# Kernel tuning notes

Measured on AMD Instinct MI355X. Metric: run time of the kernel, lower is better.

The kernel has to match this reference:

```python
import jax, jax.numpy as jnp
import numpy as np

# Config mirroring pooler_config / set_config
INPUT_LEN = 8192
POOLED_LEN = 512
DEPTH = 4            # log2(INPUT_LEN / POOLED_LEN)
BASE = 2.0           # base > 0 branch
FLIP_RIGHT = True
SORT_BACK = True
EMB_DEPTH = 768
BATCH = 8


def _pool_one(emb, score):
    """emb: [L, E], score: [L] -> ([L/2**DEPTH, E], [L/2**DEPTH]).
    One iterative sort-fold-merge chain (the per-batch our_topk)."""
    for _ in range(DEPTH):
        half = score.shape[0] // 2
        # descending sort indices (torch sort(descending=True).indices)
        sort_idx = jnp.argsort(-score)
        left = sort_idx[:half]
        right = sort_idx[half:]
        if FLIP_RIGHT:
            right = right[::-1]
        pairs = jnp.stack([left, right])            # [2, half]
        sc = score[pairs]                           # [2, half]
        # softmax over the pair dimension of base**score
        w = jax.nn.softmax(jnp.power(BASE, sc), axis=0)  # [2, half]
        score = (sc * w).sum(axis=0)                # [half]
        emb = (emb[pairs] * w[:, :, None]).sum(axis=0)   # [half, E]
        if SORT_BACK:
            # reorder merged tokens back to original order of the top (left) indices
            order = jnp.argsort(left)
            score = score[order]
            emb = emb[order]
    return emb, score


def setup_inputs() -> dict:
    key = jax.random.key(0)
    k1, k2 = jax.random.split(key)
    embs = jax.random.normal(k1, (BATCH, INPUT_LEN, EMB_DEPTH), dtype=jnp.float32)
    scores = jax.random.normal(k2, (BATCH, INPUT_LEN, 1), dtype=jnp.float32)
    return {"embs": embs, "scores": scores}


def reference(embs, scores):
    # inputs already at INPUT_LEN, so pad_to_input_len is an identity;
    # scores is squeezed from [B, L, 1] to [B, L]
    new_embs, new_scores = jax.vmap(_pool_one)(embs, scores[..., 0])
    return new_embs, new_scores
```

## Files before the change

kernel.cpp:

```cpp
#include <hip/hip_runtime.h>
#include <stdint.h>

#define BATCH   8
#define LEN0    8192
#define EMB     768
#define POOLED  512
#define NJC     16
#define PL      (BATCH * LEN0)

struct __align__(16) Rec { uint32_t iA, iB; float w0, w1; };


__device__ __forceinline__ float npy_expf(float x) {
    const float q = rintf(__fmul_rn(x, 1.44269504088896341f));
    float r = __fmaf_rn(q, -0.693359375f, x);
    r = __fmaf_rn(q, 2.12194440e-4f, r);
    const float r2 = __fmul_rn(r, r);
    float p = 1.9875691500E-4f;
    p = __fmaf_rn(p, r, 1.3981999507E-3f);
    p = __fmaf_rn(p, r, 8.3334519073E-3f);
    p = __fmaf_rn(p, r, 4.1665795894E-2f);
    p = __fmaf_rn(p, r, 1.6666665459E-1f);
    p = __fmaf_rn(p, r, 5.0000001201E-1f);
    p = __fmaf_rn(p, r2, r);
    p = __fadd_rn(p, 1.0f);
    const int qi = (int)q;
    const float sc = __uint_as_float((uint32_t)((qi + 127) << 23));
    return __fmul_rn(p, sc);
}

__global__ __launch_bounds__(256) void k_rank(const float* __restrict__ sc,
                                              uint16_t* __restrict__ rankp,
                                              int L, int C) {
    __shared__ float keys[512];
    const int b     = blockIdx.z;
    const int jc    = blockIdx.y;
    const int base  = b * LEN0;
    const int ibase = blockIdx.x * 1024;
    const int jb    = jc * C;
    const int tid   = threadIdx.x;

    for (int j = tid; j < C; j += 256)
        keys[j] = sc[base + jb + j];
    __syncthreads();

    const int i0 = ibase + tid * 4;
    const float4 mev = *(const float4*)&sc[base + i0];
    const float me[4] = {mev.x, mev.y, mev.z, mev.w};
    uint32_t cnt[4] = {0, 0, 0, 0};
    if (jb + C <= ibase) {
        for (int j = 0; j < C; j += 4) {
            const float4 kv = *(const float4*)&keys[j];
            #pragma unroll
            for (int m = 0; m < 4; m++)
                cnt[m] += (kv.x >= me[m]) + (kv.y >= me[m]) +
                          (kv.z >= me[m]) + (kv.w >= me[m]);
        }
    } else if (jb >= ibase + 1024) {
        for (int j = 0; j < C; j += 4) {
            const float4 kv = *(const float4*)&keys[j];
            #pragma unroll
            for (int m = 0; m < 4; m++)
                cnt[m] += (kv.x > me[m]) + (kv.y > me[m]) +
                          (kv.z > me[m]) + (kv.w > me[m]);
        }
    } else {
        for (int j = 0; j < C; j += 4) {
            const float4 kv = *(const float4*)&keys[j];
            const int jj = jb + j;
            #pragma unroll
            for (int m = 0; m < 4; m++) {
                const int i = i0 + m;
                cnt[m] += ((kv.x > me[m]) || (kv.x == me[m] && (jj    ) < i))
                        + ((kv.y > me[m]) || (kv.y == me[m] && (jj + 1) < i))
                        + ((kv.z > me[m]) || (kv.z == me[m] && (jj + 2) < i))
                        + ((kv.w > me[m]) || (kv.w == me[m] && (jj + 3) < i));
            }
        }
    }
    *(ushort4*)&rankp[(size_t)jc * PL + base + i0] =
        make_ushort4((uint16_t)cnt[0], (uint16_t)cnt[1],
                     (uint16_t)cnt[2], (uint16_t)cnt[3]);
}

__global__ __launch_bounds__(256) void k_sumscatter(const uint16_t* __restrict__ rankp,
                                                    uint16_t* __restrict__ rank16,
                                                    uint16_t* __restrict__ ior16,
                                                    uint32_t* __restrict__ csum,
                                                    int L) {
    __shared__ uint32_t part[256];
    const int b    = blockIdx.y;
    const int base = b * LEN0;
    const int c    = blockIdx.x;
    const int tid  = threadIdx.x;
    const int i    = c * 256 + tid;

    uint32_t r = 0;
    #pragma unroll
    for (int pl = 0; pl < NJC; pl++)
        r += rankp[(size_t)pl * PL + base + i];
    rank16[base + i] = (uint16_t)r;
    ior16[base + r] = (uint16_t)i;

    const uint32_t half = (uint32_t)(L / 2);
    uint32_t flag = (r < half) ? 1u : 0u;
    part[tid] = flag;
    __syncthreads();
    for (int off = 128; off > 0; off >>= 1) {
        if (tid < off) part[tid] += part[tid + off];
        __syncthreads();
    }
    if (tid == 0) csum[b * 32 + c] = part[0];
}

__global__ __launch_bounds__(256) void k_pairx(const float* __restrict__ sc_cur,
                                               float* __restrict__ sc_nxt,
                                               const uint16_t* __restrict__ rank16,
                                               const uint16_t* __restrict__ ior16,
                                               const uint32_t* __restrict__ csum,
                                               Rec* __restrict__ rec,
                                               int L) {
    __shared__ uint32_t cs[32];
    __shared__ uint32_t part[256];
    const int b    = blockIdx.y;
    const int base = b * LEN0;
    const int c    = blockIdx.x;
    const int tid  = threadIdx.x;
    const int i    = c * 256 + tid;
    const uint32_t half = (uint32_t)(L / 2);

    if (tid < c) cs[tid] = csum[b * 32 + tid];
    const uint32_t r = rank16[base + i];
    const uint32_t flag = (r < half) ? 1u : 0u;
    part[tid] = flag;
    __syncthreads();

    uint32_t dstBase = 0;
    for (int t = 0; t < c; t++) dstBase += cs[t];

    for (int off = 1; off < 256; off <<= 1) {
        uint32_t v = part[tid];
        uint32_t add = (tid >= off) ? part[tid - off] : 0u;
        __syncthreads();
        part[tid] = v + add;
        __syncthreads();
    }
    if (!flag) return;
    const uint32_t dst = dstBase + part[tid] - 1u;

    const uint32_t p = ior16[base + (uint32_t)(L - 1) - r];
    const float s0 = sc_cur[base + i];
    const float s1 = sc_cur[base + p];
    const float p0 = (float)exp2((double)s0);
    const float p1 = (float)exp2((double)s1);
    const float mx = fmaxf(p0, p1);
    const float d0 = __fsub_rn(p0, mx);
    const float d1 = __fsub_rn(p1, mx);
    const float e0 = npy_expf(d0);
    const float e1 = npy_expf(d1);
    const float den = __fadd_rn(e0, e1);
    const float w0 = __fdiv_rn(e0, den);
    const float w1 = __fdiv_rn(e1, den);
    sc_nxt[base + dst] = __fadd_rn(__fmul_rn(s0, w0), __fmul_rn(s1, w1));

    Rec rc; rc.iA = (uint32_t)i; rc.iB = p; rc.w0 = w0; rc.w1 = w1;
    rec[(size_t)b * half + dst] = rc;
}

__global__ __launch_bounds__(192)
void k_merge(const float* __restrict__ emb,
             const Rec* __restrict__ rec0, const Rec* __restrict__ rec1,
             const Rec* __restrict__ rec2, const Rec* __restrict__ rec3,
             const float* __restrict__ sc_fin, float* __restrict__ out) {
    __shared__ uint32_t sl[2][16];
    __shared__ float    sw[2][16];
    const int s = blockIdx.x;
    const int b = blockIdx.y;
    const int d = threadIdx.x;

    if (d == 0) {
        const Rec r = rec3[b * 512 + s];
        sl[0][0] = r.iA; sl[0][1] = r.iB;
        sw[0][0] = r.w0; sw[0][1] = r.w1;
    }
    __syncthreads();
    if (d < 2) {
        const Rec r = rec2[b * 1024 + sl[0][d]];
        sl[1][2*d] = r.iA; sl[1][2*d+1] = r.iB;
        sw[1][2*d]   = __fmul_rn(sw[0][d], r.w0);
        sw[1][2*d+1] = __fmul_rn(sw[0][d], r.w1);
    }
    __syncthreads();
    if (d < 4) {
        const Rec r = rec1[b * 2048 + sl[1][d]];
        sl[0][2*d] = r.iA; sl[0][2*d+1] = r.iB;
        sw[0][2*d]   = __fmul_rn(sw[1][d], r.w0);
        sw[0][2*d+1] = __fmul_rn(sw[1][d], r.w1);
    }
    __syncthreads();
    if (d < 8) {
        const Rec r = rec0[b * 4096 + sl[0][d]];
        sl[1][2*d] = r.iA; sl[1][2*d+1] = r.iB;
        sw[1][2*d]   = __fmul_rn(sw[0][d], r.w0);
        sw[1][2*d+1] = __fmul_rn(sw[0][d], r.w1);
    }
    __syncthreads();

    const float* ebase = emb + (size_t)b * LEN0 * EMB;
    float4 acc = make_float4(0.f, 0.f, 0.f, 0.f);
    #pragma unroll
    for (int k = 0; k < 16; k++) {
        const float4 v = *(const float4*)(ebase + (size_t)sl[1][k] * EMB + d * 4);
        const float wk = sw[1][k];
        acc.x += wk * v.x; acc.y += wk * v.y; acc.z += wk * v.z; acc.w += wk * v.w;
    }
    *(float4*)(out + ((size_t)b * POOLED + s) * EMB + d * 4) = acc;
    if (d == 0)
        out[(size_t)BATCH * POOLED * EMB + b * POOLED + s] = sc_fin[b * LEN0 + s];
}

extern "C" void kernel_launch(void* const* d_in, const int* in_sizes, int n_in,
                              void* d_out, int out_size, void* d_ws, size_t ws_size,
                              hipStream_t stream) {
    const float* embs   = (const float*)d_in[0];
    const float* scores = (const float*)d_in[1];
    float* out = (float*)d_out;
    char* ws = (char*)d_ws;

    float*    scA    = (float*)(ws + 0x000000);
    float*    scB    = (float*)(ws + 0x040000);
    uint16_t* rank16 = (uint16_t*)(ws + 0x080000);
    uint16_t* ior16  = (uint16_t*)(ws + 0x0A0000);
    Rec*      rec0   = (Rec*)(ws + 0x0C0000);
    Rec*      rec1   = (Rec*)(ws + 0x140000);
    Rec*      rec2   = (Rec*)(ws + 0x180000);
    Rec*      rec3   = (Rec*)(ws + 0x1A0000);
    uint16_t* rankp  = (uint16_t*)(ws + 0x1C0000);
    uint32_t* csum   = (uint32_t*)(ws + 0x3C0000);

    const float* sc_in[4]  = {scores, scA, scB, scA};
    float*       sc_out[4] = {scA, scB, scA, scB};
    Rec*         recs[4]   = {rec0, rec1, rec2, rec3};

    int L = LEN0;
    for (int l = 0; l < 4; l++) {
        const int C = L / NJC;
        k_rank<<<dim3(L / 1024, NJC, BATCH), 256, 0, stream>>>(sc_in[l], rankp, L, C);
        k_sumscatter<<<dim3(L / 256, BATCH), 256, 0, stream>>>(rankp, rank16, ior16, csum, L);
        k_pairx<<<dim3(L / 256, BATCH), 256, 0, stream>>>(sc_in[l], sc_out[l],
                                                          rank16, ior16, csum, recs[l], L);
        L >>= 1;
    }

    k_merge<<<dim3(POOLED, BATCH), 192, 0, stream>>>(embs, rec0, rec1, rec2, rec3,
                                                     scB, out);
}
```

Measured before the change: 177.0 us.

## Fuse rank counting and sum-scatter into one full-row shared-memory kernel

Replaces the split rank-partial kernel plus the separate summation/scatter kernel with a templated kernel per level. Each 1024-thread block loads the whole score row into LDS, splits the comparison work across thread groups, and reduces the partial counts in shared memory before writing rank, inverse index and chunk sums. This removes the global rankp round trip and one launch per level. The cost is a redundant full-row load per block, a large LDS footprint that limits occupancy, and a fixed grid of 32 blocks per batch at every level.

```diff
diff --git a/kernel.cpp b/kernel.cpp
--- a/kernel.cpp
+++ b/kernel.cpp
@@ -5,8 +5,6 @@
 #define LEN0    8192
 #define EMB     768
 #define POOLED  512
-#define NJC     16
-#define PL      (BATCH * LEN0)
 
 struct __align__(16) Rec { uint32_t iA, iB; float w0, w1; };
 
@@ -29,35 +27,45 @@
     return __fmul_rn(p, sc);
 }
 
-__global__ __launch_bounds__(256) void k_rank(const float* __restrict__ sc,
-                                              uint16_t* __restrict__ rankp,
-                                              int L, int C) {
-    __shared__ float keys[512];
-    const int b     = blockIdx.z;
-    const int jc    = blockIdx.y;
+template<int L>
+__global__ __launch_bounds__(1024) void k_rankfull(const float* __restrict__ sc,
+                                                   uint16_t* __restrict__ rank16,
+                                                   uint16_t* __restrict__ ior16,
+                                                   uint32_t* __restrict__ csum) {
+    constexpr int IC = L / 32;
+    constexpr int IQ = IC / 4;
+    constexpr int G  = 1024 / IQ;
+    constexpr int JR = L / G;
+    __shared__ float    keys[L];
+    __shared__ uint16_t partial[4096];
+    __shared__ uint32_t wsum[16];
+    const int b     = blockIdx.y;
     const int base  = b * LEN0;
-    const int ibase = blockIdx.x * 1024;
-    const int jb    = jc * C;
+    const int ibase = blockIdx.x * IC;
     const int tid   = threadIdx.x;
 
-    for (int j = tid; j < C; j += 256)
-        keys[j] = sc[base + jb + j];
-    __syncthreads();
-
-    const int i0 = ibase + tid * 4;
-    const float4 mev = *(const float4*)&sc[base + i0];
+    for (int e = tid * 4; e < L; e += 4096)
+        *(float4*)&keys[e] = *(const float4*)&sc[base + e];
+    __syncthreads();
+
+    const int iq  = tid % IQ;
+    const int g   = tid / IQ;
+    const int i0  = ibase + iq * 4;
+    const int jlo = g * JR;
+    const float4 mev = *(const float4*)&keys[i0];
     const float me[4] = {mev.x, mev.y, mev.z, mev.w};
+
     uint32_t cnt[4] = {0, 0, 0, 0};
-    if (jb + C <= ibase) {
-        for (int j = 0; j < C; j += 4) {
+    if (jlo + JR <= i0) {
+        for (int j = jlo; j < jlo + JR; j += 4) {
             const float4 kv = *(const float4*)&keys[j];
             #pragma unroll
             for (int m = 0; m < 4; m++)
                 cnt[m] += (kv.x >= me[m]) + (kv.y >= me[m]) +
                           (kv.z >= me[m]) + (kv.w >= me[m]);
         }
-    } else if (jb >= ibase + 1024) {
-        for (int j = 0; j < C; j += 4) {
+    } else if (jlo >= i0 + 4) {
+        for (int j = jlo; j < jlo + JR; j += 4) {
             const float4 kv = *(const float4*)&keys[j];
             #pragma unroll
             for (int m = 0; m < 4; m++)
@@ -65,52 +73,46 @@
                           (kv.z > me[m]) + (kv.w > me[m]);
         }
     } else {
-        for (int j = 0; j < C; j += 4) {
+        for (int j = jlo; j < jlo + JR; j += 4) {
             const float4 kv = *(const float4*)&keys[j];
-            const int jj = jb + j;
             #pragma unroll
             for (int m = 0; m < 4; m++) {
                 const int i = i0 + m;
-                cnt[m] += ((kv.x > me[m]) || (kv.x == me[m] && (jj    ) < i))
-                        + ((kv.y > me[m]) || (kv.y == me[m] && (jj + 1) < i))
-                        + ((kv.z > me[m]) || (kv.z == me[m] && (jj + 2) < i))
-                        + ((kv.w > me[m]) || (kv.w == me[m] && (jj + 3) < i));
+                cnt[m] += ((kv.x > me[m]) || (kv.x == me[m] && (j    ) < i))
+                        + ((kv.y > me[m]) || (kv.y == me[m] && (j + 1) < i))
+                        + ((kv.z > me[m]) || (kv.z == me[m] && (j + 2) < i))
+                        + ((kv.w > me[m]) || (kv.w == me[m] && (j + 3) < i));
             }
         }
     }
-    *(ushort4*)&rankp[(size_t)jc * PL + base + i0] =
+    *(ushort4*)&partial[g * IC + iq * 4] =
         make_ushort4((uint16_t)cnt[0], (uint16_t)cnt[1],
                      (uint16_t)cnt[2], (uint16_t)cnt[3]);
-}
-
-__global__ __launch_bounds__(256) void k_sumscatter(const uint16_t* __restrict__ rankp,
-                                                    uint16_t* __restrict__ rank16,
-                                                    uint16_t* __restrict__ ior16,
-                                                    uint32_t* __restrict__ csum,
-                                                    int L) {
-    __shared__ uint32_t part[256];
-    const int b    = blockIdx.y;
-    const int base = b * LEN0;
-    const int c    = blockIdx.x;
-    const int tid  = threadIdx.x;
-    const int i    = c * 256 + tid;
-
-    uint32_t r = 0;
+    __syncthreads();
+
+    uint32_t flag = 0;
+    if (tid < IC) {
+        uint32_t r = 0;
+        #pragma unroll 4
+        for (int gg = 0; gg < G; gg++)
+            r += partial[gg * IC + tid];
+        const int i = ibase + tid;
+        rank16[base + i] = (uint16_t)r;
+        ior16[base + r] = (uint16_t)i;
+        flag = (r < (uint32_t)(L / 2)) ? 1u : 0u;
+    }
     #pragma unroll
-    for (int pl = 0; pl < NJC; pl++)
-        r += rankp[(size_t)pl * PL + base + i];
-    rank16[base + i] = (uint16_t)r;
-    ior16[base + r] = (uint16_t)i;
-
-    const uint32_t half = (uint32_t)(L / 2);
-    uint32_t flag = (r < half) ? 1u : 0u;
-    part[tid] = flag;
-    __syncthreads();
-    for (int off = 128; off > 0; off >>= 1) {
-        if (tid < off) part[tid] += part[tid + off];
-        __syncthreads();
-    }
-    if (tid == 0) csum[b * 32 + c] = part[0];
+    for (int off = 32; off > 0; off >>= 1)
+        flag += __shfl_down(flag, off, 64);
+    if ((tid & 63) == 0) wsum[tid >> 6] = flag;
+    __syncthreads();
+    if (tid == 0) {
+        uint32_t s = 0;
+        constexpr int NW = (IC + 63) / 64;
+        #pragma unroll
+        for (int w = 0; w < NW; w++) s += wsum[w];
+        csum[b * 32 + blockIdx.x] = s;
+    }
 }
 
 __global__ __launch_bounds__(256) void k_pairx(const float* __restrict__ sc_cur,
@@ -119,7 +121,7 @@
                                                const uint16_t* __restrict__ ior16,
                                                const uint32_t* __restrict__ csum,
                                                Rec* __restrict__ rec,
-                                               int L) {
+                                               int L, int NCHPB) {
     __shared__ uint32_t cs[32];
     __shared__ uint32_t part[256];
     const int b    = blockIdx.y;
@@ -129,14 +131,15 @@
     const int i    = c * 256 + tid;
     const uint32_t half = (uint32_t)(L / 2);
 
-    if (tid < c) cs[tid] = csum[b * 32 + tid];
+    if (tid < 32) cs[tid] = csum[b * 32 + tid];
     const uint32_t r = rank16[base + i];
     const uint32_t flag = (r < half) ? 1u : 0u;
     part[tid] = flag;
     __syncthreads();
 
     uint32_t dstBase = 0;
-    for (int t = 0; t < c; t++) dstBase += cs[t];
+    const int nch = c * NCHPB;
+    for (int t = 0; t < nch; t++) dstBase += cs[t];
 
     for (int off = 1; off < 256; off <<= 1) {
         uint32_t v = part[tid];
@@ -235,22 +238,22 @@
     Rec*      rec1   = (Rec*)(ws + 0x140000);
     Rec*      rec2   = (Rec*)(ws + 0x180000);
     Rec*      rec3   = (Rec*)(ws + 0x1A0000);
-    uint16_t* rankp  = (uint16_t*)(ws + 0x1C0000);
     uint32_t* csum   = (uint32_t*)(ws + 0x3C0000);
 
-    const float* sc_in[4]  = {scores, scA, scB, scA};
-    float*       sc_out[4] = {scA, scB, scA, scB};
-    Rec*         recs[4]   = {rec0, rec1, rec2, rec3};
-
-    int L = LEN0;
-    for (int l = 0; l < 4; l++) {
-        const int C = L / NJC;
-        k_rank<<<dim3(L / 1024, NJC, BATCH), 256, 0, stream>>>(sc_in[l], rankp, L, C);
-        k_sumscatter<<<dim3(L / 256, BATCH), 256, 0, stream>>>(rankp, rank16, ior16, csum, L);
-        k_pairx<<<dim3(L / 256, BATCH), 256, 0, stream>>>(sc_in[l], sc_out[l],
-                                                          rank16, ior16, csum, recs[l], L);
-        L >>= 1;
-    }
+    const dim3 rg(32, BATCH);
+
+    k_rankfull<8192><<<rg, 1024, 0, stream>>>(scores, rank16, ior16, csum);
+    k_pairx<<<dim3(32, BATCH), 256, 0, stream>>>(scores, scA, rank16, ior16,
+                                                 csum, rec0, 8192, 1);
+    k_rankfull<4096><<<rg, 1024, 0, stream>>>(scA, rank16, ior16, csum);
+    k_pairx<<<dim3(16, BATCH), 256, 0, stream>>>(scA, scB, rank16, ior16,
+                                                 csum, rec1, 4096, 2);
+    k_rankfull<2048><<<rg, 1024, 0, stream>>>(scB, rank16, ior16, csum);
+    k_pairx<<<dim3(8, BATCH), 256, 0, stream>>>(scB, scA, rank16, ior16,
+                                                csum, rec2, 2048, 4);
+    k_rankfull<1024><<<rg, 1024, 0, stream>>>(scA, rank16, ior16, csum);
+    k_pairx<<<dim3(4, BATCH), 256, 0, stream>>>(scA, scB, rank16, ior16,
+                                                csum, rec3, 1024, 8);
 
     k_merge<<<dim3(POOLED, BATCH), 192, 0, stream>>>(embs, rec0, rec1, rec2, rec3,
                                                      scB, out);
```

Measured after the change: 146.1 us, median of 2. 1.21x faster.
